# Optimization experiments

Measured on AMD Instinct MI355X. Metric: run time of the kernel, lower is better.

Reference implementation:

```python
import jax, jax.numpy as jnp
import numpy as np

IN_FEATURES = 4096
OUT_FEATURES = 4096
NNZ = 1677721  # int(4096*4096*(1-0.9))


def setup_inputs() -> dict:
    key = jax.random.key(0)
    k1, k2, k3, k4 = jax.random.split(key, 4)
    x = jax.random.normal(k1, (4, 2048, IN_FEATURES), dtype=jnp.float32)
    bound = 1.0 / np.sqrt(IN_FEATURES)
    sparse_values = jax.random.uniform(k2, (NNZ,), minval=-bound, maxval=bound, dtype=jnp.float32)
    bias = jax.random.uniform(k3, (OUT_FEATURES,), minval=-bound, maxval=bound, dtype=jnp.float32)
    flat_idx = jnp.sort(jax.random.randint(k4, (NNZ,), 0, IN_FEATURES * OUT_FEATURES, dtype=jnp.int64))
    return {"x": x, "sparse_values": sparse_values, "bias": bias, "flat_idx": flat_idx}


def reference(x, sparse_values, bias, flat_idx):
    # Fixed COO pattern: row = flat // in_features, col = flat % in_features
    rows = flat_idx // IN_FEATURES
    cols = flat_idx % IN_FEATURES
    # Scatter-add == COO coalesce (duplicates summed). W: [out, in]
    W = jnp.zeros((OUT_FEATURES, IN_FEATURES), dtype=sparse_values.dtype).at[rows, cols].add(sparse_values)
    # y = x W^T + b  (matches torch.sparse.mm(W, x^T)^T + b)
    y = jnp.einsum('bsi,oi->bso', x, W) + bias
    return y.astype(x.dtype)
```

## Files before the change

### kernel.cpp

```cpp
#include <hip/hip_runtime.h>
#include <hip/hip_bf16.h>
#include <stdint.h>

#define IN_F 4096
#define OUT_F 4096

typedef __attribute__((ext_vector_type(8))) __bf16 bf16x8;
typedef __attribute__((ext_vector_type(4))) float f32x4;

__device__ __forceinline__ void gl_lds_16(const void* g, void* l) {
    __builtin_amdgcn_global_load_lds((const __attribute__((address_space(1))) void*)g,
                                     (__attribute__((address_space(3))) void*)l,
                                     16, 0, 0);
}

__global__ void cvt_x(const float* __restrict__ x, __bf16* __restrict__ Xb, int n8) {
    int i = blockIdx.x * blockDim.x + threadIdx.x;
    if (i < n8) {
        const float4* src = (const float4*)(x + (size_t)i * 8);
        float4 v0 = src[0], v1 = src[1];
        bf16x8 o;
        o[0] = (__bf16)v0.x; o[1] = (__bf16)v0.y; o[2] = (__bf16)v0.z; o[3] = (__bf16)v0.w;
        o[4] = (__bf16)v1.x; o[5] = (__bf16)v1.y; o[6] = (__bf16)v1.z; o[7] = (__bf16)v1.w;
        *(bf16x8*)(Xb + (size_t)i * 8) = o;
    }
}

__global__ void scatter_w(const float* __restrict__ vals, const int* __restrict__ idx,
                          __bf16* __restrict__ W, int nnz) {
    int i = blockIdx.x * blockDim.x + threadIdx.x;
    if (i >= nnz) return;
    const int id = idx[i];
    if (i > 0 && idx[i - 1] == id) return;
    float s = vals[i];
    for (int j = i + 1; j < nnz && idx[j] == id; ++j) s += vals[j];
    W[id] = (__bf16)s;
}

#define BM 256
#define BN 256
#define BK 32
#define NT (IN_F / BK)

__global__ __launch_bounds__(512, 2) void gemm_bf16_bt(
    const __bf16* __restrict__ A, const __bf16* __restrict__ B,
    const float* __restrict__ bias, float* __restrict__ C,
    int M, int N, int K)
{
    __shared__ __align__(128) __bf16 lds[4][16384];

    const int t512 = threadIdx.x;
    const int wave = t512 >> 6;
    const int lane = t512 & 63;
    const int wm = wave >> 2;
    const int wn = wave & 3;
    const int lq = lane >> 4;
    const int lr = lane & 15;

    const int bid  = blockIdx.x;
    const int wgid = (bid & 7) * 64 + (bid >> 3);
    const int mt = wgid >> 4;
    const int nt = wgid & 15;
    const int tileM = mt * BM;
    const int tileN = nt * BN;

    const int srow = t512 >> 2;
    const int scol = ((t512 & 3) ^ ((t512 >> 3) & 3)) * 8;

    const __bf16* gA0 = A + (size_t)(tileM + srow) * K + scol;
    const __bf16* gA1 = A + (size_t)(tileM + 128 + srow) * K + scol;
    const __bf16* gB0 = B + (size_t)(tileN + srow) * K + scol;
    const __bf16* gB1 = B + (size_t)(tileN + 128 + srow) * K + scol;

#define STAGE_A(buf, k0) do { \
        gl_lds_16(gA0 + (k0), &lds[buf][0]    + t512 * 8); \
        gl_lds_16(gA1 + (k0), &lds[buf][4096] + t512 * 8); } while (0)
#define STAGE_B(buf, k0) do { \
        gl_lds_16(gB0 + (k0), &lds[buf][8192]         + t512 * 8); \
        gl_lds_16(gB1 + (k0), &lds[buf][8192 + 4096]  + t512 * 8); } while (0)

    const int cswz = (lq ^ ((lr >> 1) & 3)) * 8;
    const int aoff = (wm * 128 + lr) * BK + cswz;
    const int boff = 8192 + (wn * 64 + lr) * BK + cswz;

    f32x4 acc[8][4] = {};
    bf16x8 fa0[8], fb0[4], fa1[8], fb1[4];

#define MM2(FAc, FBc, MI0, MI1) do {                                            \
        _Pragma("unroll") for (int ni_ = 0; ni_ < 4; ++ni_)                     \
            acc[MI0][ni_] = __builtin_amdgcn_mfma_f32_16x16x32_bf16(            \
                FAc[MI0], FBc[ni_], acc[MI0][ni_], 0, 0, 0);                    \
        _Pragma("unroll") for (int ni_ = 0; ni_ < 4; ++ni_)                     \
            acc[MI1][ni_] = __builtin_amdgcn_mfma_f32_16x16x32_bf16(            \
                FAc[MI1], FBc[ni_], acc[MI1][ni_], 0, 0, 0);                    \
    } while (0)

#define TILE_MAIN(T, FAc, FBc, FAn, FBn) do {                                   \
        const int t_ = (T);                                                     \
        const int pb_ = (t_ + 3) & 3; const int pk_ = (t_ + 3) * BK;            \
        const __bf16* nb_ = &lds[(t_ + 1) & 3][0];                              \
                                                  \
        STAGE_A(pb_, pk_);                                                      \
        FAn[0] = *(const bf16x8*)&nb_[aoff];                                    \
        FAn[1] = *(const bf16x8*)&nb_[aoff + 512];                              \
        FBn[0] = *(const bf16x8*)&nb_[boff];                                    \
        MM2(FAc, FBc, 0, 1);                                                    \
                                                  \
        STAGE_B(pb_, pk_);                                                      \
        FBn[1] = *(const bf16x8*)&nb_[boff + 512];                              \
        FBn[2] = *(const bf16x8*)&nb_[boff + 1024];                             \
        FBn[3] = *(const bf16x8*)&nb_[boff + 1536];                             \
        MM2(FAc, FBc, 2, 3);                                                    \
                                                          \
        FAn[2] = *(const bf16x8*)&nb_[aoff + 1024];                             \
        FAn[3] = *(const bf16x8*)&nb_[aoff + 1536];                             \
        FAn[4] = *(const bf16x8*)&nb_[aoff + 2048];                             \
        MM2(FAc, FBc, 4, 5);                                                    \
                                                          \
        FAn[5] = *(const bf16x8*)&nb_[aoff + 2560];                             \
        FAn[6] = *(const bf16x8*)&nb_[aoff + 3072];                             \
        FAn[7] = *(const bf16x8*)&nb_[aoff + 3584];                             \
        MM2(FAc, FBc, 6, 7);                                                    \
           \
        __builtin_amdgcn_sched_group_barrier(0x030, 2, 0);         \
        __builtin_amdgcn_sched_group_barrier(0x100, 3, 0);         \
        __builtin_amdgcn_sched_group_barrier(0x008, 8, 0);         \
        __builtin_amdgcn_sched_group_barrier(0x030, 2, 0);                      \
        __builtin_amdgcn_sched_group_barrier(0x100, 3, 0);                      \
        __builtin_amdgcn_sched_group_barrier(0x008, 8, 0);                      \
        __builtin_amdgcn_sched_group_barrier(0x100, 3, 0);                      \
        __builtin_amdgcn_sched_group_barrier(0x008, 8, 0);                      \
        __builtin_amdgcn_sched_group_barrier(0x100, 3, 0);                      \
        __builtin_amdgcn_sched_group_barrier(0x008, 8, 0);                      \
        asm volatile("s_waitcnt vmcnt(4)" ::: "memory");                        \
        __builtin_amdgcn_s_barrier();                                           \
        asm volatile("" ::: "memory");                                          \
    } while (0)

#define TILE(T, FAc, FBc, FAn, FBn) do {                                        \
        const int t_ = (T);                                                     \
        if (t_ + 3 < NT) {                                                      \
            const int pb_ = (t_ + 3) & 3; const int pk_ = (t_ + 3) * BK;        \
            STAGE_A(pb_, pk_); STAGE_B(pb_, pk_);                               \
        }                                                                       \
        if (t_ + 1 < NT) {                                                      \
            const __bf16* nb_ = &lds[(t_ + 1) & 3][0];                          \
            _Pragma("unroll") for (int mi = 0; mi < 8; ++mi)                    \
                FAn[mi] = *(const bf16x8*)&nb_[aoff + mi * 512];                \
            _Pragma("unroll") for (int ni = 0; ni < 4; ++ni)                    \
                FBn[ni] = *(const bf16x8*)&nb_[boff + ni * 512];                \
        }                                                                       \
        _Pragma("unroll") for (int mi = 0; mi < 8; ++mi)                        \
            _Pragma("unroll") for (int ni = 0; ni < 4; ++ni)                    \
                acc[mi][ni] = __builtin_amdgcn_mfma_f32_16x16x32_bf16(          \
                    FAc[mi], FBc[ni], acc[mi][ni], 0, 0, 0);                    \
        if (t_ < NT - 3)       asm volatile("s_waitcnt vmcnt(4)" ::: "memory"); \
        else if (t_ == NT - 3) asm volatile("s_waitcnt vmcnt(0)" ::: "memory"); \
        if (t_ < NT - 1) {                                                      \
            __builtin_amdgcn_s_barrier();                                       \
            asm volatile("" ::: "memory");                                      \
        }                                                                       \
    } while (0)

    STAGE_A(0, 0);   STAGE_B(0, 0);
    STAGE_A(1, 32);  STAGE_B(1, 32);
    STAGE_A(2, 64);  STAGE_B(2, 64);
    asm volatile("s_waitcnt vmcnt(4)" ::: "memory");
    __builtin_amdgcn_s_barrier();
    asm volatile("" ::: "memory");
    {
        const __bf16* nb_ = &lds[0][0];
#pragma unroll
        for (int mi = 0; mi < 8; ++mi) fa0[mi] = *(const bf16x8*)&nb_[aoff + mi * 512];
#pragma unroll
        for (int ni = 0; ni < 4; ++ni) fb0[ni] = *(const bf16x8*)&nb_[boff + ni * 512];
    }

    for (int t = 0; t < 124; t += 2) {
        TILE_MAIN(t,     fa0, fb0, fa1, fb1);
        TILE_MAIN(t + 1, fa1, fb1, fa0, fb0);
    }
    TILE(124, fa0, fb0, fa1, fb1);
    TILE(125, fa1, fb1, fa0, fb0);
    TILE(126, fa0, fb0, fa1, fb1);
    TILE(127, fa1, fb1, fa0, fb0);

    float bv[4];
#pragma unroll
    for (int ni = 0; ni < 4; ++ni) bv[ni] = bias[tileN + wn * 64 + ni * 16 + lr];
#pragma unroll
    for (int mi = 0; mi < 8; ++mi) {
#pragma unroll
        for (int ni = 0; ni < 4; ++ni) {
            const int gn = tileN + wn * 64 + ni * 16 + lr;
#pragma unroll
            for (int r = 0; r < 4; ++r) {
                const int gm = tileM + wm * 128 + mi * 16 + lq * 4 + r;
                C[(size_t)gm * N + gn] = acc[mi][ni][r] + bv[ni];
            }
        }
    }
#undef TILE
#undef TILE_MAIN
#undef MM2
#undef STAGE_A
#undef STAGE_B
}

extern "C" void kernel_launch(void* const* d_in, const int* in_sizes, int n_in,
                              void* d_out, int out_size, void* d_ws, size_t ws_size,
                              hipStream_t stream) {
    const float* x    = (const float*)d_in[0];
    const float* vals = (const float*)d_in[1];
    const float* bias = (const float*)d_in[2];
    const int*   idx  = (const int*)d_in[3];
    float* out = (float*)d_out;

    const int nnz = in_sizes[1];
    const int K = IN_F, N = OUT_F;
    const int M = in_sizes[0] / K;

    char* ws = (char*)d_ws;
    __bf16* Wb = (__bf16*)ws;
    __bf16* Xb = (__bf16*)(ws + (size_t)32 * 1024 * 1024);

    const int wElems = N * K;
    const int xElems = M * K;
    const int n8 = xElems / 8;
    const int cvtBlocks = n8 / 256;
    const int scatBlocks = (nnz + 255) / 256;

    hipMemsetAsync(Wb, 0, (size_t)wElems * sizeof(__bf16), stream);
    cvt_x<<<cvtBlocks, 256, 0, stream>>>(x, Xb, n8);
    scatter_w<<<scatBlocks, 256, 0, stream>>>(vals, idx, Wb, nnz);

    gemm_bf16_bt<<<(M / BM) * (N / BN), 512, 0, stream>>>(Xb, Wb, bias, out, M, N, K);
}
```

Baseline: 453.5 us.

## Fuse x conversion with dense W build via binary search, drop memset

After: 493.8 us. +8.9%, slower.

```diff
diff --git a/kernel.cpp b/kernel.cpp
--- a/kernel.cpp
+++ b/kernel.cpp
@@ -14,27 +14,34 @@
                                      16, 0, 0);
 }
 
-__global__ void cvt_x(const float* __restrict__ x, __bf16* __restrict__ Xb, int n8) {
-    int i = blockIdx.x * blockDim.x + threadIdx.x;
-    if (i < n8) {
-        const float4* src = (const float4*)(x + (size_t)i * 8);
-        float4 v0 = src[0], v1 = src[1];
+__global__ void cvt_and_build(const float* __restrict__ x, __bf16* __restrict__ Xb, int n8,
+                              const float* __restrict__ vals, const int* __restrict__ idx,
+                              __bf16* __restrict__ W, int nnz, int cvtBlocks) {
+    if ((int)blockIdx.x < cvtBlocks) {
+        int i = blockIdx.x * blockDim.x + threadIdx.x;
+        if (i < n8) {
+            const float4* src = (const float4*)(x + (size_t)i * 8);
+            float4 v0 = src[0], v1 = src[1];
+            bf16x8 o;
+            o[0] = (__bf16)v0.x; o[1] = (__bf16)v0.y; o[2] = (__bf16)v0.z; o[3] = (__bf16)v0.w;
+            o[4] = (__bf16)v1.x; o[5] = (__bf16)v1.y; o[6] = (__bf16)v1.z; o[7] = (__bf16)v1.w;
+            *(bf16x8*)(Xb + (size_t)i * 8) = o;
+        }
+    } else {
+        const int b = (int)blockIdx.x - cvtBlocks;
+        const int ts = (b << 11) + (int)threadIdx.x * 8;
+        int lo = 0, hi = nnz;
+        while (lo < hi) { int m = (lo + hi) >> 1; if (idx[m] < ts) lo = m + 1; else hi = m; }
+        int j = lo;
         bf16x8 o;
-        o[0] = (__bf16)v0.x; o[1] = (__bf16)v0.y; o[2] = (__bf16)v0.z; o[3] = (__bf16)v0.w;
-        o[4] = (__bf16)v1.x; o[5] = (__bf16)v1.y; o[6] = (__bf16)v1.z; o[7] = (__bf16)v1.w;
-        *(bf16x8*)(Xb + (size_t)i * 8) = o;
-    }
-}
-
-__global__ void scatter_w(const float* __restrict__ vals, const int* __restrict__ idx,
-                          __bf16* __restrict__ W, int nnz) {
-    int i = blockIdx.x * blockDim.x + threadIdx.x;
-    if (i >= nnz) return;
-    const int id = idx[i];
-    if (i > 0 && idx[i - 1] == id) return;
-    float s = vals[i];
-    for (int j = i + 1; j < nnz && idx[j] == id; ++j) s += vals[j];
-    W[id] = (__bf16)s;
+#pragma unroll
+        for (int k = 0; k < 8; ++k) {
+            float a = 0.0f;
+            while (j < nnz && idx[j] == ts + k) { a += vals[j]; ++j; }
+            o[k] = (__bf16)a;
+        }
+        *(bf16x8*)(W + ts) = o;
+    }
 }
 
 #define BM 256
@@ -228,11 +235,10 @@
     const int xElems = M * K;
     const int n8 = xElems / 8;
     const int cvtBlocks = n8 / 256;
-    const int scatBlocks = (nnz + 255) / 256;
-
-    hipMemsetAsync(Wb, 0, (size_t)wElems * sizeof(__bf16), stream);
-    cvt_x<<<cvtBlocks, 256, 0, stream>>>(x, Xb, n8);
-    scatter_w<<<scatBlocks, 256, 0, stream>>>(vals, idx, Wb, nnz);
+    const int buildBlocks = wElems / 2048;
+
+    cvt_and_build<<<cvtBlocks + buildBlocks, 256, 0, stream>>>(
+        x, Xb, n8, vals, idx, Wb, nnz, cvtBlocks);
 
     gemm_bf16_bt<<<(M / BM) * (N / BN), 512, 0, stream>>>(Xb, Wb, bias, out, M, N, K);
 }
```

## Fuse fp32-to-bf16 conversion of X into GEMM A-tile staging via registers

Applied to the files above, without the earlier changes.

Measured after the change: 654.9 us. 44.4% more time.

```diff
diff --git a/kernel.cpp b/kernel.cpp
--- a/kernel.cpp
+++ b/kernel.cpp
@@ -12,18 +12,6 @@
     __builtin_amdgcn_global_load_lds((const __attribute__((address_space(1))) void*)g,
                                      (__attribute__((address_space(3))) void*)l,
                                      16, 0, 0);
-}
-
-__global__ void cvt_x(const float* __restrict__ x, __bf16* __restrict__ Xb, int n8) {
-    int i = blockIdx.x * blockDim.x + threadIdx.x;
-    if (i < n8) {
-        const float4* src = (const float4*)(x + (size_t)i * 8);
-        float4 v0 = src[0], v1 = src[1];
-        bf16x8 o;
-        o[0] = (__bf16)v0.x; o[1] = (__bf16)v0.y; o[2] = (__bf16)v0.z; o[3] = (__bf16)v0.w;
-        o[4] = (__bf16)v1.x; o[5] = (__bf16)v1.y; o[6] = (__bf16)v1.z; o[7] = (__bf16)v1.w;
-        *(bf16x8*)(Xb + (size_t)i * 8) = o;
-    }
 }
 
 __global__ void scatter_w(const float* __restrict__ vals, const int* __restrict__ idx,
@@ -43,7 +31,7 @@
 #define NT (IN_F / BK)
 
 __global__ __launch_bounds__(512, 2) void gemm_bf16_bt(
-    const __bf16* __restrict__ A, const __bf16* __restrict__ B,
+    const float* __restrict__ X, const __bf16* __restrict__ B,
     const float* __restrict__ bias, float* __restrict__ C,
     int M, int N, int K)
 {
@@ -67,24 +55,37 @@
     const int srow = t512 >> 2;
     const int scol = ((t512 & 3) ^ ((t512 >> 3) & 3)) * 8;
 
-    const __bf16* gA0 = A + (size_t)(tileM + srow) * K + scol;
-    const __bf16* gA1 = A + (size_t)(tileM + 128 + srow) * K + scol;
+    const float*  gx0 = X + (size_t)(tileM + srow) * K + scol;
+    const float*  gx1 = X + (size_t)(tileM + 128 + srow) * K + scol;
     const __bf16* gB0 = B + (size_t)(tileN + srow) * K + scol;
     const __bf16* gB1 = B + (size_t)(tileN + 128 + srow) * K + scol;
 
-#define STAGE_A(buf, k0) do { \
-        gl_lds_16(gA0 + (k0), &lds[buf][0]    + t512 * 8); \
-        gl_lds_16(gA1 + (k0), &lds[buf][4096] + t512 * 8); } while (0)
 #define STAGE_B(buf, k0) do { \
         gl_lds_16(gB0 + (k0), &lds[buf][8192]         + t512 * 8); \
         gl_lds_16(gB1 + (k0), &lds[buf][8192 + 4096]  + t512 * 8); } while (0)
 
+#define LOADA(R, k0) do { \
+        R##a = *(const float4*)(gx0 + (k0)); \
+        R##b = *(const float4*)(gx0 + (k0) + 4); \
+        R##c = *(const float4*)(gx1 + (k0)); \
+        R##d = *(const float4*)(gx1 + (k0) + 4); } while (0)
+
+#define WRITEA(R, wb) do { \
+        bf16x8 w0_, w1_; \
+        w0_[0]=(__bf16)R##a.x; w0_[1]=(__bf16)R##a.y; w0_[2]=(__bf16)R##a.z; w0_[3]=(__bf16)R##a.w; \
+        w0_[4]=(__bf16)R##b.x; w0_[5]=(__bf16)R##b.y; w0_[6]=(__bf16)R##b.z; w0_[7]=(__bf16)R##b.w; \
+        w1_[0]=(__bf16)R##c.x; w1_[1]=(__bf16)R##c.y; w1_[2]=(__bf16)R##c.z; w1_[3]=(__bf16)R##c.w; \
+        w1_[4]=(__bf16)R##d.x; w1_[5]=(__bf16)R##d.y; w1_[6]=(__bf16)R##d.z; w1_[7]=(__bf16)R##d.w; \
+        *(bf16x8*)(&lds[wb][0]    + t512 * 8) = w0_; \
+        *(bf16x8*)(&lds[wb][4096] + t512 * 8) = w1_; } while (0)
+
     const int cswz = (lq ^ ((lr >> 1) & 3)) * 8;
     const int aoff = (wm * 128 + lr) * BK + cswz;
     const int boff = 8192 + (wn * 64 + lr) * BK + cswz;
 
     f32x4 acc[8][4] = {};
     bf16x8 fa0[8], fb0[4], fa1[8], fb1[4];
+    float4 r0a, r0b, r0c, r0d, r1a, r1b, r1c, r1d;
 
 #define MM2(FAc, FBc, MI0, MI1) do {                                            \
         _Pragma("unroll") for (int ni_ = 0; ni_ < 4; ++ni_)                     \
@@ -95,54 +96,53 @@
                 FAc[MI1], FBc[ni_], acc[MI1][ni_], 0, 0, 0);                    \
     } while (0)
 
-#define TILE_MAIN(T, FAc, FBc, FAn, FBn) do {                                   \
+#define TILE_MAIN(T, FAc, FBc, FAn, FBn, Rl, Rw) do {                           \
         const int t_ = (T);                                                     \
-        const int pb_ = (t_ + 3) & 3; const int pk_ = (t_ + 3) * BK;            \
+        const int pk_ = (t_ + 3) * BK;                                          \
+        const int pb_ = (t_ + 3) & 3;                                           \
+        const int wb_ = (t_ + 2) & 3;                                           \
         const __bf16* nb_ = &lds[(t_ + 1) & 3][0];                              \
-                                                  \
-        STAGE_A(pb_, pk_);                                                      \
+        LOADA(Rl, pk_);                                             \
+        STAGE_B(pb_, pk_);                                          \
+        WRITEA(Rw, wb_);                             \
         FAn[0] = *(const bf16x8*)&nb_[aoff];                                    \
         FAn[1] = *(const bf16x8*)&nb_[aoff + 512];                              \
         FBn[0] = *(const bf16x8*)&nb_[boff];                                    \
         MM2(FAc, FBc, 0, 1);                                                    \
-                                                  \
-        STAGE_B(pb_, pk_);                                                      \
         FBn[1] = *(const bf16x8*)&nb_[boff + 512];                              \
         FBn[2] = *(const bf16x8*)&nb_[boff + 1024];                             \
         FBn[3] = *(const bf16x8*)&nb_[boff + 1536];                             \
         MM2(FAc, FBc, 2, 3);                                                    \
-                                                          \
         FAn[2] = *(const bf16x8*)&nb_[aoff + 1024];                             \
         FAn[3] = *(const bf16x8*)&nb_[aoff + 1536];                             \
         FAn[4] = *(const bf16x8*)&nb_[aoff + 2048];                             \
         MM2(FAc, FBc, 4, 5);                                                    \
-                                                          \
         FAn[5] = *(const bf16x8*)&nb_[aoff + 2560];                             \
         FAn[6] = *(const bf16x8*)&nb_[aoff + 3072];                             \
         FAn[7] = *(const bf16x8*)&nb_[aoff + 3584];                             \
-        MM2(FAc, FBc, 6, 7);                                                    \
-           \
-        __builtin_amdgcn_sched_group_barrier(0x030, 2, 0);         \
-        __builtin_amdgcn_sched_group_barrier(0x100, 3, 0);         \
-        __builtin_amdgcn_sched_group_barrier(0x008, 8, 0);         \
-        __builtin_amdgcn_sched_group_barrier(0x030, 2, 0);                      \
+        __builtin_amdgcn_sched_group_barrier(0x030, 4, 0);      \
+        __builtin_amdgcn_sched_group_barrier(0x030, 2, 0);      \
+        __builtin_amdgcn_sched_group_barrier(0x200, 2, 0);      \
+        __builtin_amdgcn_sched_group_barrier(0x100, 3, 0);      \
+        __builtin_amdgcn_sched_group_barrier(0x008, 8, 0);      \
         __builtin_amdgcn_sched_group_barrier(0x100, 3, 0);                      \
         __builtin_amdgcn_sched_group_barrier(0x008, 8, 0);                      \
         __builtin_amdgcn_sched_group_barrier(0x100, 3, 0);                      \
         __builtin_amdgcn_sched_group_barrier(0x008, 8, 0);                      \
         __builtin_amdgcn_sched_group_barrier(0x100, 3, 0);                      \
+         \
+        asm volatile("s_waitcnt vmcnt(6)" ::: "memory");                        \
+        MM2(FAc, FBc, 6, 7);                                                    \
         __builtin_amdgcn_sched_group_barrier(0x008, 8, 0);                      \
-        asm volatile("s_waitcnt vmcnt(4)" ::: "memory");                        \
+        asm volatile("s_waitcnt lgkmcnt(0)" ::: "memory");                      \
         __builtin_amdgcn_s_barrier();                                           \
         asm volatile("" ::: "memory");                                          \
     } while (0)
 
-#define TILE(T, FAc, FBc, FAn, FBn) do {                                        \
+#define TILE_TAIL(T, FAc, FBc, FAn, FBn, Rl, Rw) do {                           \
         const int t_ = (T);                                                     \
-        if (t_ + 3 < NT) {                                                      \
-            const int pb_ = (t_ + 3) & 3; const int pk_ = (t_ + 3) * BK;        \
-            STAGE_A(pb_, pk_); STAGE_B(pb_, pk_);                               \
-        }                                                                       \
+        if (t_ + 3 < NT) { LOADA(Rl, (t_ + 3) * BK); STAGE_B((t_ + 3) & 3, (t_ + 3) * BK); } \
+        if (t_ + 2 < NT) { WRITEA(Rw, (t_ + 2) & 3); }                          \
         if (t_ + 1 < NT) {                                                      \
             const __bf16* nb_ = &lds[(t_ + 1) & 3][0];                          \
             _Pragma("unroll") for (int mi = 0; mi < 8; ++mi)                    \
@@ -154,18 +154,22 @@
             _Pragma("unroll") for (int ni = 0; ni < 4; ++ni)                    \
                 acc[mi][ni] = __builtin_amdgcn_mfma_f32_16x16x32_bf16(          \
                     FAc[mi], FBc[ni], acc[mi][ni], 0, 0, 0);                    \
-        if (t_ < NT - 3)       asm volatile("s_waitcnt vmcnt(4)" ::: "memory"); \
-        else if (t_ == NT - 3) asm volatile("s_waitcnt vmcnt(0)" ::: "memory"); \
+        asm volatile("s_waitcnt vmcnt(0)" ::: "memory");                        \
+        asm volatile("s_waitcnt lgkmcnt(0)" ::: "memory");                      \
         if (t_ < NT - 1) {                                                      \
             __builtin_amdgcn_s_barrier();                                       \
             asm volatile("" ::: "memory");                                      \
         }                                                                       \
     } while (0)
 
-    STAGE_A(0, 0);   STAGE_B(0, 0);
-    STAGE_A(1, 32);  STAGE_B(1, 32);
-    STAGE_A(2, 64);  STAGE_B(2, 64);
-    asm volatile("s_waitcnt vmcnt(4)" ::: "memory");
+    LOADA(r0, 0);
+    LOADA(r1, 32);
+    STAGE_B(0, 0); STAGE_B(1, 32); STAGE_B(2, 64);
+    WRITEA(r0, 0);
+    WRITEA(r1, 1);
+    LOADA(r0, 64);
+    asm volatile("s_waitcnt vmcnt(0)" ::: "memory");
+    asm volatile("s_waitcnt lgkmcnt(0)" ::: "memory");
     __builtin_amdgcn_s_barrier();
     asm volatile("" ::: "memory");
     {
@@ -177,13 +181,13 @@
     }
 
     for (int t = 0; t < 124; t += 2) {
-        TILE_MAIN(t,     fa0, fb0, fa1, fb1);
-        TILE_MAIN(t + 1, fa1, fb1, fa0, fb0);
+        TILE_MAIN(t,     fa0, fb0, fa1, fb1, r1, r0);
+        TILE_MAIN(t + 1, fa1, fb1, fa0, fb0, r0, r1);
     }
-    TILE(124, fa0, fb0, fa1, fb1);
-    TILE(125, fa1, fb1, fa0, fb0);
-    TILE(126, fa0, fb0, fa1, fb1);
-    TILE(127, fa1, fb1, fa0, fb0);
+    TILE_TAIL(124, fa0, fb0, fa1, fb1, r1, r0);
+    TILE_TAIL(125, fa1, fb1, fa0, fb0, r0, r1);
+    TILE_TAIL(126, fa0, fb0, fa1, fb1, r1, r0);
+    TILE_TAIL(127, fa1, fb1, fa0, fb0, r0, r1);
 
     float bv[4];
 #pragma unroll
@@ -200,10 +204,11 @@
             }
         }
     }
-#undef TILE
+#undef TILE_TAIL
 #undef TILE_MAIN
 #undef MM2
-#undef STAGE_A
+#undef WRITEA
+#undef LOADA
 #undef STAGE_B
 }
 
@@ -220,19 +225,12 @@
     const int K = IN_F, N = OUT_F;
     const int M = in_sizes[0] / K;
 
-    char* ws = (char*)d_ws;
-    __bf16* Wb = (__bf16*)ws;
-    __bf16* Xb = (__bf16*)(ws + (size_t)32 * 1024 * 1024);
-
+    __bf16* Wb = (__bf16*)d_ws;
     const int wElems = N * K;
-    const int xElems = M * K;
-    const int n8 = xElems / 8;
-    const int cvtBlocks = n8 / 256;
     const int scatBlocks = (nnz + 255) / 256;
 
     hipMemsetAsync(Wb, 0, (size_t)wElems * sizeof(__bf16), stream);
-    cvt_x<<<cvtBlocks, 256, 0, stream>>>(x, Xb, n8);
     scatter_w<<<scatBlocks, 256, 0, stream>>>(vals, idx, Wb, nnz);
 
-    gemm_bf16_bt<<<(M / BM) * (N / BN), 512, 0, stream>>>(Xb, Wb, bias, out, M, N, K);
-}
+    gemm_bf16_bt<<<(M / BM) * (N / BN), 512, 0, stream>>>(x, Wb, bias, out, M, N, K);
+}
```
